# Optimization experiments

Measured on AMD Instinct MI355X. Metric: run time of the kernel, lower is better.

Reference implementation:

```python
import jax, jax.numpy as jnp
import numpy as np

N_NODES = 100000
N_EDGES = 1600000
LATENT = 64
NODE_DIM = 7
EDGE_DIM = 3
N_PARAMS = 2

def asinh_layer(p, x):
    # learned asinh: a*arcsinh(b*x + c) + d, p = [a, b, c, d]
    return p[0] * jnp.arcsinh(p[1] * x + p[2]) + p[3]

def mlp2(x, w1, b1, w2, b2):
    # ExplicitMLP([L, L]): gelu between layers, none on last
    return jax.nn.gelu(x @ w1 + b1) @ w2 + b2

def agg_stats(x, n):
    # custom_aggregation: [sum, mean, var, max]; mean/var denominators are n_data
    s = jnp.sum(x, axis=0, keepdims=True)
    m = s / n
    v = jnp.sum((x - m) ** 2, axis=0, keepdims=True) / n
    mx = jnp.max(x, axis=0, keepdims=True)
    return jnp.concatenate([s, m, v, mx], axis=-1)

def _forward(nodes, edges, asinh_node, w_en, b_en, asinh_edge, w_ee, b_ee, asinh_glob, w_eg, b_eg, ew1, eb1, ew2, eb2, nw1, nb1, nw2, nb2, gw1, gb1, gw2, gb2, gw3, gb3, senders):
    # decorate_nodes=False -> zero columns 0:4
    nodes = nodes.at[:, 0:4].set(0.0)
    # globals = arcsinh([n_node, n_edge]) as (1, 2)
    glob = jnp.arcsinh(jnp.array([[float(N_NODES), float(N_EDGES)]], dtype=nodes.dtype))
    # GraphMapFeatures embedding: asinh layer + Dense for nodes/edges/globals
    nodes = asinh_layer(asinh_node, nodes) @ w_en + b_en   # (N, L)
    edges = asinh_layer(asinh_edge, edges) @ w_ee + b_ee   # (E, L)
    glob = asinh_layer(asinh_glob, glob) @ w_eg + b_eg     # (1, L)
    # source overwrites receivers with senders
    recv = senders
    # edge update: concat(edges, nodes[senders], nodes[receivers], globals)
    ge = jnp.broadcast_to(glob, (edges.shape[0], glob.shape[-1]))
    e_in = jnp.concatenate([edges, nodes[senders], nodes[recv], ge], axis=-1)  # (E, 4L)
    edges = mlp2(e_in, ew1, eb1, ew2, eb2)                                     # (E, L)
    # node update: sent/received aggregates are identical since recv == senders
    sent = jax.ops.segment_sum(edges, senders, num_segments=N_NODES)           # (N, L)
    gn = jnp.broadcast_to(glob, (nodes.shape[0], glob.shape[-1]))
    n_in = jnp.concatenate([nodes, sent, sent, gn], axis=-1)                   # (N, 4L)
    nodes = mlp2(n_in, nw1, nb1, nw2, nb2)                                     # (N, L)
    # global update: arcsinh of [sum, mean, var, max] over nodes and edges (single graph)
    node_attr = jnp.arcsinh(agg_stats(nodes, float(N_NODES)))                  # (1, 4L)
    edge_attr = jnp.arcsinh(agg_stats(edges, float(N_EDGES)))                  # (1, 4L)
    g_in = jnp.concatenate([node_attr, edge_attr, glob], axis=-1)              # (1, 9L)
    g = jax.nn.gelu(g_in @ gw1 + gb1)
    g = jax.nn.gelu(g @ gw2 + gb2)
    g = g @ gw3 + gb3
    return g.reshape(-1)  # (N_PARAMS,)

def setup_inputs():
    key = jax.random.key(0)
    ks = jax.random.split(key, 16)
    L = LATENT
    def dense(k, fi, fo):
        return jax.random.normal(k, (fi, fo), jnp.float32) / np.float32(np.sqrt(fi))
    z = lambda n: jnp.zeros((n,), jnp.float32)
    asinh0 = jnp.array([1.0, 1.0, 0.0, 0.0], jnp.float32)
    return {
        "nodes": jax.random.normal(ks[0], (N_NODES, NODE_DIM), jnp.float32),
        "edges": jax.random.normal(ks[1], (N_EDGES, EDGE_DIM), jnp.float32),
        "senders": jax.random.randint(ks[2], (N_EDGES,), 0, N_NODES),
        "asinh_node": asinh0, "w_en": dense(ks[3], NODE_DIM, L), "b_en": z(L),
        "asinh_edge": asinh0, "w_ee": dense(ks[4], EDGE_DIM, L), "b_ee": z(L),
        "asinh_glob": asinh0, "w_eg": dense(ks[5], 2, L), "b_eg": z(L),
        "ew1": dense(ks[6], 4 * L, L), "eb1": z(L),
        "ew2": dense(ks[7], L, L), "eb2": z(L),
        "nw1": dense(ks[8], 4 * L, L), "nb1": z(L),
        "nw2": dense(ks[9], L, L), "nb2": z(L),
        "gw1": dense(ks[10], 9 * L, L), "gb1": z(L),
        "gw2": dense(ks[11], L, L), "gb2": z(L),
        "gw3": dense(ks[12], L, N_PARAMS), "gb3": z(N_PARAMS),
    }

def reference(nodes, edges, senders, asinh_node, w_en, b_en, asinh_edge, w_ee, b_ee, asinh_glob, w_eg, b_eg, ew1, eb1, ew2, eb2, nw1, nb1, nw2, nb2, gw1, gb1, gw2, gb2, gw3, gb3):
    return _forward(nodes, edges, asinh_node, w_en, b_en, asinh_edge, w_ee, b_ee, asinh_glob, w_eg, b_eg, ew1, eb1, ew2, eb2, nw1, nb1, nw2, nb2, gw1, gb1, gw2, gb2, gw3, gb3, senders)
```

## Files before the change

### kernel.cpp

```cpp
#include <hip/hip_runtime.h>
#include <cstdint>
#include <cstddef>

#define NN 100000
#define NE 1600000
#define NSLICE 16
#define NBLK 782
#define NBUCK 391
#define NCHUNK 391
#define CHA 4096

#define PRE_GLOB 0
#define PRE_WC   64
#define PRE_CVEC 256
#define PRE_CN   320
#define PRE_NGV  384
#define PRE_WSR  448
#define PRE_NSR  4544

#define TAB_W2  0
#define TAB_NW1 1
#define TAB_NSR 2
#define TAB_NW2 3
#define TAB_WSR 4

typedef short v8s __attribute__((ext_vector_type(8)));
typedef float v4f __attribute__((ext_vector_type(4)));

__device__ __forceinline__ float asinhf_fast(float x){
    float ax = fabsf(x);
    float r = __logf(ax + sqrtf(fmaf(ax, ax, 1.0f)));
    return copysignf(r, x);
}
__device__ __forceinline__ float gelu_f(float x){
    float x3 = x * x * x;
    float y = 1.5957691216057308f * fmaf(0.044715f, x3, x);
    float e = __expf(y);
    float r = __builtin_amdgcn_rcpf(e + 1.0f);
    return fmaf(-x, r, x);
}
__device__ __forceinline__ unsigned fkey(float f){
    unsigned u = __float_as_uint(f);
    return (u & 0x80000000u) ? ~u : (u | 0x80000000u);
}
__device__ __forceinline__ float funkey(unsigned k){
    unsigned u = (k & 0x80000000u) ? (k ^ 0x80000000u) : ~k;
    return __uint_as_float(u);
}
__device__ __forceinline__ void atomAddF(float* p, float v){
#if defined(__HIP_DEVICE_COMPILE__)
    unsafeAtomicAdd(p, v);
#else
    atomicAdd(p, v);
#endif
}
__device__ __forceinline__ void split8(const float* x, v8s& hi, v8s& lo){
#pragma unroll
    for (int j = 0; j < 8; ++j){
        unsigned u = __float_as_uint(x[j]);
        float hf = __uint_as_float(u & 0xFFFF0000u);
        float r = x[j] - hf;
        hi[j] = (short)(u >> 16);
        lo[j] = (short)(__float_as_uint(r) >> 16);
    }
}
__device__ __forceinline__ v4f mfma3(v8s ah, v8s al, v8s bh, v8s bl, v4f acc){
    acc = __builtin_amdgcn_mfma_f32_16x16x32_bf16(al, bh, acc, 0, 0, 0);
    acc = __builtin_amdgcn_mfma_f32_16x16x32_bf16(ah, bl, acc, 0, 0, 0);
    acc = __builtin_amdgcn_mfma_f32_16x16x32_bf16(ah, bh, acc, 0, 0, 0);
    return acc;
}
__device__ __forceinline__ void fma16(float acc[4][4], float4 a, float4 b){
    float av[4] = {a.x, a.y, a.z, a.w};
    float bv[4] = {b.x, b.y, b.z, b.w};
#pragma unroll
    for (int i = 0; i < 4; ++i)
#pragma unroll
        for (int c = 0; c < 4; ++c)
            acc[i][c] = fmaf(av[i], bv[c], acc[i][c]);
}

__global__ __launch_bounds__(256) void k_pre(const float* an, const float* w_en, const float* b_en,
                      const float* ae, const float* w_ee, const float* b_ee,
                      const float* ag, const float* w_eg, const float* b_eg,
                      const float* ew1, const float* eb1,
                      const float* nw1, const float* nb1,
                      const float* ew2, const float* nw2,
                      float* pre, unsigned short* preB, int* statsZero, int* counts)
{
    __shared__ float gls[64];
    __shared__ float red[3][4][64];
    __shared__ float redc[4][64], redn[4][64];
    int t = threadIdx.x, col = t & 63, qd = t >> 6;
    for (int i = t; i < 2 * NSLICE * 192; i += 256) statsZero[i] = 0;
    {
        int4* c4 = (int4*)counts;
        int4 z = make_int4(0, 0, 0, 0);
        for (int i = t; i < NN / 4; i += 256) c4[i] = z;
    }
    for (int i = t; i < 4096; i += 256){
        pre[PRE_WSR + i] = ew1[4096 + i] + ew1[8192 + i];
        pre[PRE_NSR + i] = nw1[4096 + i] + nw1[8192 + i];
    }
    if (t < 64){
        float g0 = asinhf_fast(100000.0f);
        float g1 = asinhf_fast(1600000.0f);
        float tg0 = fmaf(ag[0], asinhf_fast(fmaf(ag[1], g0, ag[2])), ag[3]);
        float tg1 = fmaf(ag[0], asinhf_fast(fmaf(ag[1], g1, ag[2])), ag[3]);
        float gl = fmaf(tg0, w_eg[t], fmaf(tg1, w_eg[64 + t], b_eg[t]));
        pre[PRE_GLOB + t] = gl;
        gls[t] = gl;
        float tz = fmaf(an[0], asinhf_fast(an[2]), an[3]);
        pre[PRE_CN + t] = fmaf(tz, w_en[t] + w_en[64 + t] + w_en[128 + t] + w_en[192 + t], b_en[t]);
    }
    __syncthreads();
    {
        float s0 = 0.f, s1 = 0.f, s2 = 0.f, sc = 0.f, sn = 0.f;
        int jb = qd * 16;
#pragma unroll 4
        for (int j = jb; j < jb + 16; ++j){
            float e1 = ew1[j * 64 + col];
            s0 = fmaf(w_ee[j], e1, s0);
            s1 = fmaf(w_ee[64 + j], e1, s1);
            s2 = fmaf(w_ee[128 + j], e1, s2);
            sc = fmaf(b_ee[j], e1, sc);
            float g = gls[j];
            sc = fmaf(g, ew1[(192 + j) * 64 + col], sc);
            sn = fmaf(g, nw1[(192 + j) * 64 + col], sn);
        }
        red[0][qd][col] = s0; red[1][qd][col] = s1; red[2][qd][col] = s2;
        redc[qd][col] = sc; redn[qd][col] = sn;
    }
    __syncthreads();
    if (t < 64){
#pragma unroll
        for (int i = 0; i < 3; ++i)
            pre[PRE_WC + i * 64 + t] = (red[i][0][t] + red[i][1][t]) + (red[i][2][t] + red[i][3][t]);
        pre[PRE_CVEC + t] = eb1[t] + (redc[0][t] + redc[1][t]) + (redc[2][t] + redc[3][t]);
        pre[PRE_NGV + t] = nb1[t] + (redn[0][t] + redn[1][t]) + (redn[2][t] + redn[3][t]);
    }
    __syncthreads();
    const float* srcs[5] = {ew2, nw1, pre + PRE_NSR, nw2, pre + PRE_WSR};
    for (int idx = t; idx < 5 * 4096; idx += 256){
        int tab = idx >> 12;
        int rem = idx & 4095;
        int c = rem >> 10;
        int ch = (rem >> 9) & 1;
        int lane = (rem >> 3) & 63;
        int j = rem & 7;
        int k = ch * 32 + (lane >> 4) * 8 + j;
        int n = c * 16 + (lane & 15);
        float v = srcs[tab][k * 64 + n];
        unsigned u = __float_as_uint(v);
        float hf = __uint_as_float(u & 0xFFFF0000u);
        float r = v - hf;
        int base = tab * 8192 + ((c * 2 + ch) * 2) * 512 + lane * 8 + j;
        preB[base] = (unsigned short)(u >> 16);
        preB[base + 512] = (unsigned short)(__float_as_uint(r) >> 16);
    }
}

__global__ __launch_bounds__(256) void k_nproj(const float* nodes, const float* an,
                                               const float* w_en, const float* pre,
                                               const unsigned short* preB,
                                               const int* senders, int* counts,
                                               float* sent, float* nproj)
{
    __shared__ float fz[64][4];
    __shared__ float latS[64][68];
    int t = threadIdx.x;
    int base = blockIdx.x * 64;
    int cnt = NN - base; if (cnt > 64) cnt = 64;
    const int NT = 1563 * 256;
    int gtid = blockIdx.x * 256 + t;
    for (int i = gtid; i < NE; i += NT)
        atomicAdd(&counts[senders[i]], 1);
    {
        float4 z = make_float4(0.f, 0.f, 0.f, 0.f);
        float4* s4 = (float4*)sent;
        for (int i = gtid; i < NN * 16; i += NT) s4[i] = z;
    }
    if (t < 64){
        float pa = an[0], pb = an[1], pc = an[2], pd = an[3];
        float t4 = 0.f, t5 = 0.f, t6 = 0.f;
        if (t < cnt){
            const float* row = nodes + (size_t)(base + t) * 7;
            t4 = fmaf(pa, asinhf_fast(fmaf(pb, row[4], pc)), pd);
            t5 = fmaf(pa, asinhf_fast(fmaf(pb, row[5], pc)), pd);
            t6 = fmaf(pa, asinhf_fast(fmaf(pb, row[6], pc)), pd);
        }
        fz[t][0] = t4; fz[t][1] = t5; fz[t][2] = t6;
    }
    __syncthreads();
    {
        int k = t & 63, grp = t >> 6;
        float w4 = w_en[4 * 64 + k], w5 = w_en[5 * 64 + k], w6 = w_en[6 * 64 + k];
        float cn = pre[PRE_CN + k];
#pragma unroll
        for (int i = 0; i < 16; ++i){
            int nl = grp * 16 + i;
            float v = cn;
            v = fmaf(fz[nl][0], w4, v);
            v = fmaf(fz[nl][1], w5, v);
            v = fmaf(fz[nl][2], w6, v);
            latS[nl][k] = (nl < cnt) ? v : 0.f;
        }
    }
    __syncthreads();
    int l = t & 63, w = t >> 6;
    int m = l & 15, q = l >> 4;
    v8s ah[2], al[2];
#pragma unroll
    for (int ch = 0; ch < 2; ++ch){
        float a[8];
        const float* src = &latS[w * 16 + m][ch * 32 + q * 8];
#pragma unroll
        for (int j = 0; j < 8; ++j) a[j] = src[j];
        split8(a, ah[ch], al[ch]);
    }
    const v8s* WB = (const v8s*)(preB + TAB_WSR * 8192);
    v4f acc[4];
#pragma unroll
    for (int c = 0; c < 4; ++c){
        acc[c] = (v4f){0.f, 0.f, 0.f, 0.f};
#pragma unroll
        for (int ch = 0; ch < 2; ++ch){
            v8s bh = WB[((c * 2 + ch) * 2 + 0) * 64 + l];
            v8s bl = WB[((c * 2 + ch) * 2 + 1) * 64 + l];
            acc[c] = mfma3(ah[ch], al[ch], bh, bl, acc[c]);
        }
    }
#pragma unroll
    for (int c = 0; c < 4; ++c)
#pragma unroll
        for (int r = 0; r < 4; ++r){
            int nl = w * 16 + q * 4 + r;
            if (nl < cnt)
                nproj[(size_t)(base + nl) * 64 + c * 16 + m] = acc[c][r];
        }
}

__global__ __launch_bounds__(128) void k_scanA(const int* counts, int* cursor, int* bsums)
{
    __shared__ int sA[128];
    int t = threadIdx.x, b = blockIdx.x;
    int i = b * 128 + t;
    int v = (i < NN) ? counts[i] : 0;
    sA[t] = v;
    __syncthreads();
    for (int off = 1; off < 128; off <<= 1){
        int x = (t >= off) ? sA[t - off] : 0;
        __syncthreads();
        sA[t] += x;
        __syncthreads();
    }
    if (i < NN) cursor[i] = sA[t] - v;
    if (t == 127) bsums[b] = sA[127];
}

__global__ __launch_bounds__(1024) void k_scanB(const int* bsums, int* bpre, int* bucketFill)
{
    __shared__ int sB[1024];
    int t = threadIdx.x;
    int v = (t < NBLK) ? bsums[t] : 0;
    sB[t] = v;
    __syncthreads();
    for (int off = 1; off < 1024; off <<= 1){
        int x = (t >= off) ? sB[t - off] : 0;
        __syncthreads();
        sB[t] += x;
        __syncthreads();
    }
    if (t < NBLK) bpre[t] = sB[t] - v;
    if (t < NBUCK) bucketFill[t] = (t == 0) ? 0 : sB[2 * t - 1];
}

__global__ __launch_bounds__(256) void k_binA(const float* edges, const int* senders,
                                              const float* ae, int* bucketFill, float4* binned)
{
    __shared__ int hist[NBUCK], hist2[NBUCK], runS[NBUCK];
    __shared__ int lofs[NBUCK + 1];
    __shared__ int sA[512];
    __shared__ int staged[CHA];
    int t = threadIdx.x, b = blockIdx.x;
    int beg = b * CHA;
    int end = beg + CHA; if (end > NE) end = NE;
    int n = end - beg;
    for (int i = t; i < NBUCK; i += 256){ hist[i] = 0; hist2[i] = 0; }
    __syncthreads();
    for (int i = beg + t; i < end; i += 256)
        atomicAdd(&hist[senders[i] >> 8], 1);
    __syncthreads();
    sA[t] = (t < NBUCK) ? hist[t] : 0;
    sA[t + 256] = (t + 256 < NBUCK) ? hist[t + 256] : 0;
    __syncthreads();
    for (int off = 1; off < 512; off <<= 1){
        int x0 = (t >= off) ? sA[t - off] : 0;
        int p = t + 256;
        int x1 = (p >= off) ? sA[p - off] : 0;
        __syncthreads();
        sA[t] += x0; sA[p] += x1;
        __syncthreads();
    }
    if (t < NBUCK) lofs[t] = sA[t] - hist[t];
    if (t + 256 < NBUCK) lofs[t + 256] = sA[t + 256] - hist[t + 256];
    if (t == 0) lofs[NBUCK] = n;
    for (int i = t; i < NBUCK; i += 256)
        if (hist[i] > 0) runS[i] = atomicAdd(&bucketFill[i], hist[i]);
    __syncthreads();
    for (int i = beg + t; i < end; i += 256){
        int bk = senders[i] >> 8;
        int r = atomicAdd(&hist2[bk], 1);
        staged[lofs[bk] + r] = i;
    }
    __syncthreads();
    float pa = ae[0], pb = ae[1], pc = ae[2], pd = ae[3];
    for (int p = t; p < n; p += 256){
        int lo = 0, hi = NBUCK;
        while (hi - lo > 1){
            int mid = (lo + hi) >> 1;
            if (lofs[mid] <= p) lo = mid; else hi = mid;
        }
        int idx = staged[p];
        const float* er = edges + (size_t)idx * 3;
        float t0 = fmaf(pa, asinhf_fast(fmaf(pb, er[0], pc)), pd);
        float t1 = fmaf(pa, asinhf_fast(fmaf(pb, er[1], pc)), pd);
        float t2 = fmaf(pa, asinhf_fast(fmaf(pb, er[2], pc)), pd);
        binned[runS[lo] + (p - lofs[lo])] =
            make_float4(t0, t1, t2, __int_as_float(senders[idx]));
    }
}

__global__ __launch_bounds__(256) void k_binB(const float4* binned, const int* cursor,
                                              const int* bpre, float4* eperm)
{
    __shared__ int cnt256[256];
    int t = threadIdx.x, b = blockIdx.x;
    int base = bpre[2 * b];
    int end = (b == NBUCK - 1) ? NE : bpre[2 * b + 2];
    cnt256[t] = 0;
    __syncthreads();
    for (int i = base + t; i < end; i += 256){
        float4 ed = binned[i];
        int s = __float_as_int(ed.w);
        int r = atomicAdd(&cnt256[s & 255], 1);
        eperm[cursor[s] + bpre[s >> 7] + r] = ed;
    }
}

__global__ __launch_bounds__(256) void k_edge_sorted(const float4* eperm, const float* nproj,
                                                     const float* pre, const unsigned short* preB,
                                                     const float* eb2,
                                                     float* sent, float* epart)
{
    __shared__ float oS[64][65];
    __shared__ float cWs[256];
    __shared__ int sArr[64];
    int t = threadIdx.x;
    cWs[t] = (t < 64) ? pre[PRE_CVEC + t] : pre[PRE_WC + t - 64];
    int l = t & 63, w = t >> 6;
    int m = l & 15, q = l >> 4;
    int e = w * 16 + m;
    float4 ed = eperm[blockIdx.x * 64 + e];
    int s = __float_as_int(ed.w);
    if (q == 0) sArr[e] = s;
    const float4* npb = (const float4*)(nproj + (size_t)s * 64);
    float4 npv0 = npb[2 * q], npv1 = npb[2 * q + 1];
    float4 npv2 = npb[8 + 2 * q], npv3 = npb[8 + 2 * q + 1];
    float t0 = ed.x, t1 = ed.y, t2 = ed.z;
    __syncthreads();
    float npf[2][8] = {{npv0.x, npv0.y, npv0.z, npv0.w, npv1.x, npv1.y, npv1.z, npv1.w},
                       {npv2.x, npv2.y, npv2.z, npv2.w, npv3.x, npv3.y, npv3.z, npv3.w}};
    v8s ah[2], al[2];
#pragma unroll
    for (int ch = 0; ch < 2; ++ch){
        int k0 = ch * 32 + q * 8;
        float h[8];
#pragma unroll
        for (int j = 0; j < 8; ++j){
            int k = k0 + j;
            float hp = cWs[k] + npf[ch][j];
            hp = fmaf(t0, cWs[64 + k], hp);
            hp = fmaf(t1, cWs[128 + k], hp);
            hp = fmaf(t2, cWs[192 + k], hp);
            h[j] = gelu_f(hp);
        }
        split8(h, ah[ch], al[ch]);
    }
    const v8s* WB = (const v8s*)(preB + TAB_W2 * 8192);
#pragma unroll
    for (int c = 0; c < 4; ++c){
        v4f acc = (v4f){0.f, 0.f, 0.f, 0.f};
#pragma unroll
        for (int ch = 0; ch < 2; ++ch){
            v8s bh = WB[((c * 2 + ch) * 2 + 0) * 64 + l];
            v8s bl = WB[((c * 2 + ch) * 2 + 1) * 64 + l];
            acc = mfma3(ah[ch], al[ch], bh, bl, acc);
        }
        float bb = eb2[c * 16 + m];
#pragma unroll
        for (int r = 0; r < 4; ++r)
            oS[w * 16 + q * 4 + r][c * 16 + m] = acc[r] + bb;
    }
    __syncthreads();
    if (w == 0){
        int k = l;
        int cur = sArr[0];
        int jstart = 0;
        float a = 0.f;
        for (int j = 0; j < 64; ++j){
            int sj = sArr[j];
            if (sj != cur){
                float* dst = sent + (size_t)cur * 64 + k;
                if (jstart > 0) *dst = a; else atomAddF(dst, a);
                cur = sj; a = 0.f; jstart = j;
            }
            a += oS[j][k];
        }
        atomAddF(sent + (size_t)cur * 64 + k, a);
    } else if (w == 1){
        int k = l;
        float ssum = 0.f, qsum = 0.f, mmax = -INFINITY;
#pragma unroll 4
        for (int j = 0; j < 64; ++j){
            float v = oS[j][k];
            ssum += v;
            qsum = fmaf(v, v, qsum);
            mmax = fmaxf(mmax, v);
        }
        float* ep = epart + (size_t)(blockIdx.x & (NSLICE - 1)) * 192;
        atomAddF(ep + k, ssum);
        atomAddF(ep + 64 + k, qsum);
        atomicMax((unsigned*)(ep + 128) + k, fkey(mmax));
    }
}

__global__ __launch_bounds__(256) void k_edge_atomic(const float* edges, const int* senders,
                                                     const float* nproj, const float* pre,
                                                     const float* ae, const float* ew2, const float* eb2,
                                                     float* sent, float* epart)
{
    __shared__ float hT[64][68];
    __shared__ int sArr[64];
    int t = threadIdx.x;
    int e = t & 63, kq = t >> 6;
    int eg = blockIdx.x * 64 + e;
    int s = senders[eg];
    if (kq == 0) sArr[e] = s;
    float pa = ae[0], pb = ae[1], pc = ae[2], pd = ae[3];
    const float* erow = edges + (size_t)eg * 3;
    float t0 = fmaf(pa, asinhf_fast(fmaf(pb, erow[0], pc)), pd);
    float t1 = fmaf(pa, asinhf_fast(fmaf(pb, erow[1], pc)), pd);
    float t2 = fmaf(pa, asinhf_fast(fmaf(pb, erow[2], pc)), pd);
    int j0 = kq * 16;
    const float* np = nproj + (size_t)s * 64 + j0;
    float npv[16];
#pragma unroll
    for (int qq = 0; qq < 4; ++qq){
        float4 v = *(const float4*)(np + qq * 4);
        npv[qq * 4 + 0] = v.x; npv[qq * 4 + 1] = v.y; npv[qq * 4 + 2] = v.z; npv[qq * 4 + 3] = v.w;
    }
    const float* Wc = pre + PRE_WC;
    const float* cvec = pre + PRE_CVEC;
#pragma unroll
    for (int jj = 0; jj < 16; ++jj){
        int j = j0 + jj;
        float hp = cvec[j] + npv[jj];
        hp = fmaf(t0, Wc[j], hp);
        hp = fmaf(t1, Wc[64 + j], hp);
        hp = fmaf(t2, Wc[128 + j], hp);
        hT[j][e] = gelu_f(hp);
    }
    __syncthreads();
    int e0 = (t & 15) * 4, k0 = (t >> 4) * 4;
    float acc[4][4];
    {
        float4 bb = *(const float4*)(eb2 + k0);
#pragma unroll
        for (int i = 0; i < 4; ++i){ acc[i][0] = bb.x; acc[i][1] = bb.y; acc[i][2] = bb.z; acc[i][3] = bb.w; }
    }
#pragma unroll 4
    for (int j = 0; j < 64; ++j){
        float4 a = *(const float4*)&hT[j][e0];
        float4 b = *(const float4*)(ew2 + j * 64 + k0);
        fma16(acc, a, b);
    }
#pragma unroll
    for (int i = 0; i < 4; ++i){
        int sv = sArr[e0 + i];
        float* dst = sent + (size_t)sv * 64 + k0;
        atomAddF(dst + 0, acc[i][0]);
        atomAddF(dst + 1, acc[i][1]);
        atomAddF(dst + 2, acc[i][2]);
        atomAddF(dst + 3, acc[i][3]);
    }
    float ps[4], pq[4], pm[4];
#pragma unroll
    for (int c = 0; c < 4; ++c){
        float s0 = acc[0][c], s1 = acc[1][c], s2 = acc[2][c], s3 = acc[3][c];
        ps[c] = (s0 + s1) + (s2 + s3);
        pq[c] = fmaf(s0, s0, fmaf(s1, s1, fmaf(s2, s2, s3 * s3)));
        pm[c] = fmaxf(fmaxf(s0, s1), fmaxf(s2, s3));
    }
#pragma unroll
    for (int msk = 1; msk < 16; msk <<= 1){
#pragma unroll
        for (int c = 0; c < 4; ++c){
            ps[c] += __shfl_xor(ps[c], msk);
            pq[c] += __shfl_xor(pq[c], msk);
            pm[c] = fmaxf(pm[c], __shfl_xor(pm[c], msk));
        }
    }
    float* ep = epart + (size_t)(blockIdx.x & (NSLICE - 1)) * 192;
    if ((t & 15) == 0){
#pragma unroll
        for (int c = 0; c < 4; ++c){
            atomAddF(ep + k0 + c, ps[c]);
            atomAddF(ep + 64 + k0 + c, pq[c]);
            atomicMax((unsigned*)(ep + 128) + k0 + c, fkey(pm[c]));
        }
    }
}

__global__ __launch_bounds__(256) void k_node(const float* nodes, const float* an,
                                              const float* w_en, const float* sent,
                                              const float* pre, const unsigned short* preB,
                                              const float* nb2, float* npart)
{
    __shared__ float fz[64][4];
    __shared__ float h2S[64][68];
    __shared__ float sS[4][64], qS[4][64], mS[4][64];
    int t = threadIdx.x;
    int base = blockIdx.x * 64;
    int cnt = NN - base; if (cnt > 64) cnt = 64;
    if (t < 64){
        float pa = an[0], pb = an[1], pc = an[2], pd = an[3];
        float t4 = 0.f, t5 = 0.f, t6 = 0.f;
        if (t < cnt){
            const float* row = nodes + (size_t)(base + t) * 7;
            t4 = fmaf(pa, asinhf_fast(fmaf(pb, row[4], pc)), pd);
            t5 = fmaf(pa, asinhf_fast(fmaf(pb, row[5], pc)), pd);
            t6 = fmaf(pa, asinhf_fast(fmaf(pb, row[6], pc)), pd);
        }
        fz[t][0] = t4; fz[t][1] = t5; fz[t][2] = t6;
    }
    __syncthreads();
    int l = t & 63, w = t >> 6;
    int m = l & 15, q = l >> 4;
    int rowA = w * 16 + m;
    bool vA = rowA < cnt;
    float f0 = fz[rowA][0], f1 = fz[rowA][1], f2 = fz[rowA][2];
    v8s lh[2], ll[2], sh[2], sl[2];
#pragma unroll
    for (int ch = 0; ch < 2; ++ch){
        int k0 = ch * 32 + q * 8;
        float a[8], b[8] = {0,0,0,0,0,0,0,0};
#pragma unroll
        for (int j = 0; j < 8; ++j){
            int k = k0 + j;
            float v = pre[PRE_CN + k];
            v = fmaf(f0, w_en[4 * 64 + k], v);
            v = fmaf(f1, w_en[5 * 64 + k], v);
            v = fmaf(f2, w_en[6 * 64 + k], v);
            a[j] = vA ? v : 0.f;
        }
        if (vA){
            const float4* psn = (const float4*)(sent + (size_t)(base + rowA) * 64 + k0);
            float4 b0 = psn[0], b1 = psn[1];
            b[0]=b0.x; b[1]=b0.y; b[2]=b0.z; b[3]=b0.w; b[4]=b1.x; b[5]=b1.y; b[6]=b1.z; b[7]=b1.w;
        }
        split8(a, lh[ch], ll[ch]);
        split8(b, sh[ch], sl[ch]);
    }
    const v8s* B1 = (const v8s*)(preB + TAB_NW1 * 8192);
    const v8s* BS = (const v8s*)(preB + TAB_NSR * 8192);
    v4f acc[4];
#pragma unroll
    for (int c = 0; c < 4; ++c){
        acc[c] = (v4f){0.f, 0.f, 0.f, 0.f};
#pragma unroll
        for (int ch = 0; ch < 2; ++ch){
            v8s bh = B1[((c * 2 + ch) * 2 + 0) * 64 + l];
            v8s bl = B1[((c * 2 + ch) * 2 + 1) * 64 + l];
            acc[c] = mfma3(lh[ch], ll[ch], bh, bl, acc[c]);
            v8s ch2 = BS[((c * 2 + ch) * 2 + 0) * 64 + l];
            v8s cl2 = BS[((c * 2 + ch) * 2 + 1) * 64 + l];
// ... 11 lines not shown
        float a[8];
        const float* src = &h2S[w * 16 + m][ch * 32 + q * 8];
#pragma unroll
        for (int j = 0; j < 8; ++j) a[j] = src[j];
        split8(a, ah[ch], al[ch]);
    }
    const v8s* B2 = (const v8s*)(preB + TAB_NW2 * 8192);
    float ps[4], pq[4], pm[4];
#pragma unroll
    for (int c = 0; c < 4; ++c){
        v4f a2 = (v4f){0.f, 0.f, 0.f, 0.f};
#pragma unroll
        for (int ch = 0; ch < 2; ++ch){
            v8s bh = B2[((c * 2 + ch) * 2 + 0) * 64 + l];
            v8s bl = B2[((c * 2 + ch) * 2 + 1) * 64 + l];
            a2 = mfma3(ah[ch], al[ch], bh, bl, a2);
        }
        float bb = nb2[c * 16 + m];
        ps[c] = 0.f; pq[c] = 0.f; pm[c] = -INFINITY;
#pragma unroll
        for (int r = 0; r < 4; ++r){
            int nl = w * 16 + q * 4 + r;
            if (nl < cnt){
                float v = a2[r] + bb;
                ps[c] += v;
                pq[c] = fmaf(v, v, pq[c]);
                pm[c] = fmaxf(pm[c], v);
            }
        }
    }
#pragma unroll
    for (int msk = 16; msk <= 32; msk <<= 1){
#pragma unroll
        for (int c = 0; c < 4; ++c){
            ps[c] += __shfl_xor(ps[c], msk);
            pq[c] += __shfl_xor(pq[c], msk);
            pm[c] = fmaxf(pm[c], __shfl_xor(pm[c], msk));
        }
    }
    if (l < 16){
#pragma unroll
        for (int c = 0; c < 4; ++c){
            sS[w][c * 16 + l] = ps[c];
            qS[w][c * 16 + l] = pq[c];
            mS[w][c * 16 + l] = pm[c];
        }
    }
    __syncthreads();
    if (t < 64){
        int k = t;
        float ssum = sS[0][k] + sS[1][k] + sS[2][k] + sS[3][k];
        float qsum = qS[0][k] + qS[1][k] + qS[2][k] + qS[3][k];
        float mmax = fmaxf(fmaxf(mS[0][k], mS[1][k]), fmaxf(mS[2][k], mS[3][k]));
        float* np = npart + (size_t)(blockIdx.x & (NSLICE - 1)) * 192;
        atomAddF(np + k, ssum);
        atomAddF(np + 64 + k, qsum);
        atomicMax((unsigned*)(np + 128) + k, fkey(mmax));
    }
}

__global__ __launch_bounds__(256) void k_final(const float* pre, const float* epart, const float* npart,
                        const float* gw1, const float* gb1, const float* gw2, const float* gb2,
                        const float* gw3, const float* gb3, float* out)
{
    __shared__ float gin[576];
    __shared__ float p1[4][64];
    __shared__ float l1s[64];
    __shared__ float l2s[64];
    int t = threadIdx.x;
    if (t < 64){
        float ns = 0.f, nq = 0.f; unsigned nmk = 0u;
        float es = 0.f, eq = 0.f; unsigned emk = 0u;
        for (int sl = 0; sl < NSLICE; ++sl){
            const float* np = npart + (size_t)sl * 192;
            const float* ep = epart + (size_t)sl * 192;
            ns += np[t]; nq += np[64 + t];
            unsigned a = ((const unsigned*)(np + 128))[t]; if (a > nmk) nmk = a;
            es += ep[t]; eq += ep[64 + t];
            unsigned b = ((const unsigned*)(ep + 128))[t]; if (b > emk) emk = b;
        }
        float mean = ns / 100000.0f;
        float var = nq / 100000.0f - mean * mean;
        gin[t] = asinhf_fast(ns);
        gin[64 + t] = asinhf_fast(mean);
        gin[128 + t] = asinhf_fast(var);
        gin[192 + t] = asinhf_fast(funkey(nmk));
        float meane = es / 1600000.0f;
        float vare = eq / 1600000.0f - meane * meane;
        gin[256 + t] = asinhf_fast(es);
        gin[320 + t] = asinhf_fast(meane);
        gin[384 + t] = asinhf_fast(vare);
        gin[448 + t] = asinhf_fast(funkey(emk));
        gin[512 + t] = pre[PRE_GLOB + t];
    }
    __syncthreads();
    {
        int col = t & 63, qq = t >> 6;
        float a1 = 0.f;
        for (int j = qq * 144; j < qq * 144 + 144; ++j)
            a1 = fmaf(gin[j], gw1[j * 64 + col], a1);
        p1[qq][col] = a1;
    }
    __syncthreads();
    if (t < 64){
        float a = gb1[t] + ((p1[0][t] + p1[1][t]) + (p1[2][t] + p1[3][t]));
        l1s[t] = gelu_f(a);
    }
    __syncthreads();
    if (t < 64){
        float a2 = gb2[t];
        for (int j = 0; j < 64; ++j) a2 = fmaf(l1s[j], gw2[j * 64 + t], a2);
        l2s[t] = gelu_f(a2);
    }
    __syncthreads();
    if (t < 2){
        float s = gb3[t];
        for (int j = 0; j < 64; ++j) s = fmaf(l2s[j], gw3[j * 2 + t], s);
        out[t] = s;
    }
}

extern "C" void kernel_launch(void* const* d_in, const int* in_sizes, int n_in,
                              void* d_out, int out_size, void* d_ws, size_t ws_size,
                              hipStream_t stream)
{
    const float* nodes  = (const float*)d_in[0];
    const float* edges  = (const float*)d_in[1];
    const int*   senders= (const int*)d_in[2];
    const float* an  = (const float*)d_in[3];
    const float* w_en= (const float*)d_in[4];
    const float* b_en= (const float*)d_in[5];
    const float* ae  = (const float*)d_in[6];
    const float* w_ee= (const float*)d_in[7];
    const float* b_ee= (const float*)d_in[8];
    const float* ag  = (const float*)d_in[9];
    const float* w_eg= (const float*)d_in[10];
    const float* b_eg= (const float*)d_in[11];
    const float* ew1 = (const float*)d_in[12];
    const float* eb1 = (const float*)d_in[13];
    const float* ew2 = (const float*)d_in[14];
    const float* eb2 = (const float*)d_in[15];
    const float* nw1 = (const float*)d_in[16];
    const float* nb1 = (const float*)d_in[17];
    const float* nw2 = (const float*)d_in[18];
    const float* nb2 = (const float*)d_in[19];
    const float* gw1 = (const float*)d_in[20];
    const float* gb1 = (const float*)d_in[21];
    const float* gw2 = (const float*)d_in[22];
    const float* gb2 = (const float*)d_in[23];
    const float* gw3 = (const float*)d_in[24];
    const float* gb3 = (const float*)d_in[25];

    char* ws = (char*)d_ws;
    float4* eperm = (float4*)(ws);
    float*  nproj = (float*)(ws + 25600000);
    float*  sent  = (float*)(ws + 51200000);
    float*  pre   = (float*)(ws + 76800000);
    unsigned short* preB = (unsigned short*)(ws + 76865536);
    float*  epart = (float*)(ws + 76963840);
    float*  npart = (float*)(ws + 76976128);
    int*    counts= (int*)  (ws + 76988416);
    int*    cursor= (int*)  (ws + 77388416);
    int*    bsums = (int*)  (ws + 77788416);
    int*    bpre  = (int*)  (ws + 77792512);
    int*    bucketFill = (int*)(ws + 77796608);
    float4* binned= (float4*)(ws + 77798416);

    const size_t NEED_FAST = 103398416;
    bool fast = (ws_size >= NEED_FAST);

    hipLaunchKernelGGL(k_pre, dim3(1), dim3(256), 0, stream,
                       an, w_en, b_en, ae, w_ee, b_ee, ag, w_eg, b_eg, ew1, eb1,
                       nw1, nb1, ew2, nw2, pre, preB, (int*)epart, counts);

    if (fast){
        hipLaunchKernelGGL(k_nproj, dim3((NN + 63) / 64), dim3(256), 0, stream,
                           nodes, an, w_en, pre, preB, senders, counts, sent, nproj);
        hipLaunchKernelGGL(k_scanA, dim3(NBLK), dim3(128), 0, stream, counts, cursor, bsums);
        hipLaunchKernelGGL(k_scanB, dim3(1), dim3(1024), 0, stream, bsums, bpre, bucketFill);
        hipLaunchKernelGGL(k_binA, dim3(NCHUNK), dim3(256), 0, stream,
                           edges, senders, ae, bucketFill, binned);
        hipLaunchKernelGGL(k_binB, dim3(NBUCK), dim3(256), 0, stream,
                           binned, cursor, bpre, eperm);
        hipLaunchKernelGGL(k_edge_sorted, dim3(NE / 64), dim3(256), 0, stream,
                           eperm, nproj, pre, preB, eb2, sent, epart);
    } else {
        hipLaunchKernelGGL(k_nproj, dim3((NN + 63) / 64), dim3(256), 0, stream,
                           nodes, an, w_en, pre, preB, senders, cursor, sent, nproj);
        hipLaunchKernelGGL(k_edge_atomic, dim3(NE / 64), dim3(256), 0, stream,
                           edges, senders, nproj, pre, ae, ew2, eb2, sent, epart);
    }

    hipLaunchKernelGGL(k_node, dim3((NN + 63) / 64), dim3(256), 0, stream,
                       nodes, an, w_en, sent, pre, preB, nb2, npart);
    hipLaunchKernelGGL(k_final, dim3(1), dim3(256), 0, stream,
                       pre, epart, npart, gw1, gb1, gw2, gb2, gw3, gb3, (float*)d_out);
}
```

Measured before the change: 429.8 us.

## Replace full counting sort with fixed-capacity 128-node buckets and LDS accumulation

Removes the per-node count, the two scan kernels and the second binning pass. Edges are instead binned straight into fixed-capacity buckets of 128 sender nodes, with a global overflow buffer for any excess. Each bucket block runs the edge MLP and accumulates the aggregated sums into shared memory with atomics, then writes its node rows of sent directly, so sent no longer needs zeroing. This cuts kernel launches and global passes over the edges. The costs are LDS atomic contention, only 782 blocks of larger per-block work, and a slow scalar fallback kernel for overflow edges.

```diff
diff --git a/kernel.cpp b/kernel.cpp
--- a/kernel.cpp
+++ b/kernel.cpp
@@ -5,10 +5,12 @@
 #define NN 100000
 #define NE 1600000
 #define NSLICE 16
-#define NBLK 782
-#define NBUCK 391
+#define NBUCK 782
+#define NBPAD 784
+#define BCAP 3072
 #define NCHUNK 391
 #define CHA 4096
+#define OVCAP 8192
 
 #define PRE_GLOB 0
 #define PRE_WC   64
@@ -86,18 +88,16 @@
                       const float* ew1, const float* eb1,
                       const float* nw1, const float* nb1,
                       const float* ew2, const float* nw2,
-                      float* pre, unsigned short* preB, int* statsZero, int* counts)
+                      float* pre, unsigned short* preB, int* statsZero,
+                      int* bucketFill, int* ovCnt)
 {
     __shared__ float gls[64];
     __shared__ float red[3][4][64];
     __shared__ float redc[4][64], redn[4][64];
     int t = threadIdx.x, col = t & 63, qd = t >> 6;
     for (int i = t; i < 2 * NSLICE * 192; i += 256) statsZero[i] = 0;
-    {
-        int4* c4 = (int4*)counts;
-        int4 z = make_int4(0, 0, 0, 0);
-        for (int i = t; i < NN / 4; i += 256) c4[i] = z;
-    }
+    for (int i = t; i < NBPAD; i += 256) bucketFill[i] = i * BCAP;
+    if (t == 0) ovCnt[0] = 0;
     for (int i = t; i < 4096; i += 256){
         pre[PRE_WSR + i] = ew1[4096 + i] + ew1[8192 + i];
         pre[PRE_NSR + i] = nw1[4096 + i] + nw1[8192 + i];
@@ -162,24 +162,13 @@
 
 __global__ __launch_bounds__(256) void k_nproj(const float* nodes, const float* an,
                                                const float* w_en, const float* pre,
-                                               const unsigned short* preB,
-                                               const int* senders, int* counts,
-                                               float* sent, float* nproj)
+                                               const unsigned short* preB, float* nproj)
 {
     __shared__ float fz[64][4];
     __shared__ float latS[64][68];
     int t = threadIdx.x;
     int base = blockIdx.x * 64;
     int cnt = NN - base; if (cnt > 64) cnt = 64;
-    const int NT = 1563 * 256;
-    int gtid = blockIdx.x * 256 + t;
-    for (int i = gtid; i < NE; i += NT)
-        atomicAdd(&counts[senders[i]], 1);
-    {
-        float4 z = make_float4(0.f, 0.f, 0.f, 0.f);
-        float4* s4 = (float4*)sent;
-        for (int i = gtid; i < NN * 16; i += NT) s4[i] = z;
-    }
     if (t < 64){
         float pa = an[0], pb = an[1], pc = an[2], pd = an[3];
         float t4 = 0.f, t5 = 0.f, t6 = 0.f;
@@ -240,83 +229,59 @@
         }
 }
 
-__global__ __launch_bounds__(128) void k_scanA(const int* counts, int* cursor, int* bsums)
-{
-    __shared__ int sA[128];
-    int t = threadIdx.x, b = blockIdx.x;
-    int i = b * 128 + t;
-    int v = (i < NN) ? counts[i] : 0;
-    sA[t] = v;
-    __syncthreads();
-    for (int off = 1; off < 128; off <<= 1){
-        int x = (t >= off) ? sA[t - off] : 0;
-        __syncthreads();
-        sA[t] += x;
-        __syncthreads();
-    }
-    if (i < NN) cursor[i] = sA[t] - v;
-    if (t == 127) bsums[b] = sA[127];
-}
-
-__global__ __launch_bounds__(1024) void k_scanB(const int* bsums, int* bpre, int* bucketFill)
-{
-    __shared__ int sB[1024];
-    int t = threadIdx.x;
-    int v = (t < NBLK) ? bsums[t] : 0;
-    sB[t] = v;
-    __syncthreads();
-    for (int off = 1; off < 1024; off <<= 1){
-        int x = (t >= off) ? sB[t - off] : 0;
-        __syncthreads();
-        sB[t] += x;
-        __syncthreads();
-    }
-    if (t < NBLK) bpre[t] = sB[t] - v;
-    if (t < NBUCK) bucketFill[t] = (t == 0) ? 0 : sB[2 * t - 1];
-}
-
 __global__ __launch_bounds__(256) void k_binA(const float* edges, const int* senders,
-                                              const float* ae, int* bucketFill, float4* binned)
-{
-    __shared__ int hist[NBUCK], hist2[NBUCK], runS[NBUCK];
-    __shared__ int lofs[NBUCK + 1];
-    __shared__ int sA[512];
+                                              const float* ae, int* bucketFill,
+                                              float4* binned, int* ovCnt, float4* ovBuf)
+{
+    __shared__ int hist[NBPAD], hist2[NBPAD], runS[NBPAD];
+    __shared__ int lofs[NBPAD + 1];
+    __shared__ int sB[256];
     __shared__ int staged[CHA];
     int t = threadIdx.x, b = blockIdx.x;
     int beg = b * CHA;
     int end = beg + CHA; if (end > NE) end = NE;
     int n = end - beg;
-    for (int i = t; i < NBUCK; i += 256){ hist[i] = 0; hist2[i] = 0; }
+    for (int i = t; i < NBPAD; i += 256){ hist[i] = 0; hist2[i] = 0; }
     __syncthreads();
     for (int i = beg + t; i < end; i += 256)
-        atomicAdd(&hist[senders[i] >> 8], 1);
-    __syncthreads();
-    sA[t] = (t < NBUCK) ? hist[t] : 0;
-    sA[t + 256] = (t + 256 < NBUCK) ? hist[t + 256] : 0;
-    __syncthreads();
-    for (int off = 1; off < 512; off <<= 1){
-        int x0 = (t >= off) ? sA[t - off] : 0;
-        int p = t + 256;
-        int x1 = (p >= off) ? sA[p - off] : 0;
+        atomicAdd(&hist[senders[i] >> 7], 1);
+    __syncthreads();
+    int i0 = 4 * t;
+    int h0 = (i0 < NBPAD) ? hist[i0] : 0;
+    int h1 = (i0 + 1 < NBPAD) ? hist[i0 + 1] : 0;
+    int h2 = (i0 + 2 < NBPAD) ? hist[i0 + 2] : 0;
+    int h3 = (i0 + 3 < NBPAD) ? hist[i0 + 3] : 0;
+    int tot = h0 + h1 + h2 + h3;
+    sB[t] = tot;
+    __syncthreads();
+    for (int off = 1; off < 256; off <<= 1){
+        int x = (t >= off) ? sB[t - off] : 0;
         __syncthreads();
-        sA[t] += x0; sA[p] += x1;
+        sB[t] += x;
         __syncthreads();
     }
-    if (t < NBUCK) lofs[t] = sA[t] - hist[t];
-    if (t + 256 < NBUCK) lofs[t + 256] = sA[t + 256] - hist[t + 256];
-    if (t == 0) lofs[NBUCK] = n;
-    for (int i = t; i < NBUCK; i += 256)
+    {
+        int run = sB[t] - tot;
+        if (i0 < NBPAD){
+            lofs[i0] = run; run += h0;
+            lofs[i0 + 1] = run; run += h1;
+            lofs[i0 + 2] = run; run += h2;
+            lofs[i0 + 3] = run;
+        }
+        if (t == 255) lofs[NBPAD] = sB[255];
+    }
+    for (int i = t; i < NBPAD; i += 256)
         if (hist[i] > 0) runS[i] = atomicAdd(&bucketFill[i], hist[i]);
     __syncthreads();
     for (int i = beg + t; i < end; i += 256){
-        int bk = senders[i] >> 8;
+        int bk = senders[i] >> 7;
         int r = atomicAdd(&hist2[bk], 1);
         staged[lofs[bk] + r] = i;
     }
     __syncthreads();
     float pa = ae[0], pb = ae[1], pc = ae[2], pd = ae[3];
     for (int p = t; p < n; p += 256){
-        int lo = 0, hi = NBUCK;
+        int lo = 0, hi = NBPAD;
         while (hi - lo > 1){
             int mid = (lo + hi) >> 1;
             if (lofs[mid] <= p) lo = mid; else hi = mid;
@@ -326,112 +291,154 @@
         float t0 = fmaf(pa, asinhf_fast(fmaf(pb, er[0], pc)), pd);
         float t1 = fmaf(pa, asinhf_fast(fmaf(pb, er[1], pc)), pd);
         float t2 = fmaf(pa, asinhf_fast(fmaf(pb, er[2], pc)), pd);
-        binned[runS[lo] + (p - lofs[lo])] =
-            make_float4(t0, t1, t2, __int_as_float(senders[idx]));
-    }
-}
-
-__global__ __launch_bounds__(256) void k_binB(const float4* binned, const int* cursor,
-                                              const int* bpre, float4* eperm)
-{
-    __shared__ int cnt256[256];
-    int t = threadIdx.x, b = blockIdx.x;
-    int base = bpre[2 * b];
-    int end = (b == NBUCK - 1) ? NE : bpre[2 * b + 2];
-    cnt256[t] = 0;
-    __syncthreads();
-    for (int i = base + t; i < end; i += 256){
-        float4 ed = binned[i];
-        int s = __float_as_int(ed.w);
-        int r = atomicAdd(&cnt256[s & 255], 1);
-        eperm[cursor[s] + bpre[s >> 7] + r] = ed;
-    }
-}
-
-__global__ __launch_bounds__(256) void k_edge_sorted(const float4* eperm, const float* nproj,
+        float4 f4 = make_float4(t0, t1, t2, __int_as_float(senders[idx]));
+        int slot = runS[lo] + (p - lofs[lo]);
+        if (slot < (lo + 1) * BCAP){
+            binned[slot] = f4;
+        } else {
+            int o = atomicAdd(ovCnt, 1);
+            if (o < OVCAP) ovBuf[o] = f4;
+        }
+    }
+}
+
+__global__ __launch_bounds__(256) void k_edge_bucket(const float4* binned, const float* nproj,
+                                                     const int* bucketFill,
                                                      const float* pre, const unsigned short* preB,
                                                      const float* eb2,
                                                      float* sent, float* epart)
 {
-    __shared__ float oS[64][65];
+    __shared__ float acc[128][65];
     __shared__ float cWs[256];
-    __shared__ int sArr[64];
-    int t = threadIdx.x;
+    __shared__ float sS[4][64], qS[4][64], mS[4][64];
+    int t = threadIdx.x, b = blockIdx.x;
+    int nodeBase = b * 128;
+    int cnt = bucketFill[b] - b * BCAP; if (cnt > BCAP) cnt = BCAP;
     cWs[t] = (t < 64) ? pre[PRE_CVEC + t] : pre[PRE_WC + t - 64];
+    for (int i = t; i < 128 * 65; i += 256) ((float*)acc)[i] = 0.f;
     int l = t & 63, w = t >> 6;
     int m = l & 15, q = l >> 4;
-    int e = w * 16 + m;
-    float4 ed = eperm[blockIdx.x * 64 + e];
-    int s = __float_as_int(ed.w);
-    if (q == 0) sArr[e] = s;
-    const float4* npb = (const float4*)(nproj + (size_t)s * 64);
-    float4 npv0 = npb[2 * q], npv1 = npb[2 * q + 1];
-    float4 npv2 = npb[8 + 2 * q], npv3 = npb[8 + 2 * q + 1];
-    float t0 = ed.x, t1 = ed.y, t2 = ed.z;
-    __syncthreads();
-    float npf[2][8] = {{npv0.x, npv0.y, npv0.z, npv0.w, npv1.x, npv1.y, npv1.z, npv1.w},
-                       {npv2.x, npv2.y, npv2.z, npv2.w, npv3.x, npv3.y, npv3.z, npv3.w}};
-    v8s ah[2], al[2];
-#pragma unroll
-    for (int ch = 0; ch < 2; ++ch){
-        int k0 = ch * 32 + q * 8;
-        float h[8];
-#pragma unroll
-        for (int j = 0; j < 8; ++j){
-            int k = k0 + j;
-            float hp = cWs[k] + npf[ch][j];
-            hp = fmaf(t0, cWs[64 + k], hp);
-            hp = fmaf(t1, cWs[128 + k], hp);
-            hp = fmaf(t2, cWs[192 + k], hp);
-            h[j] = gelu_f(hp);
-        }
-        split8(h, ah[ch], al[ch]);
-    }
+    float ps[4] = {0.f, 0.f, 0.f, 0.f}, pq[4] = {0.f, 0.f, 0.f, 0.f};
+    float pm[4] = {-INFINITY, -INFINITY, -INFINITY, -INFINITY};
+    __syncthreads();
+    const float4* bb = binned + (size_t)b * BCAP;
     const v8s* WB = (const v8s*)(preB + TAB_W2 * 8192);
-#pragma unroll
-    for (int c = 0; c < 4; ++c){
-        v4f acc = (v4f){0.f, 0.f, 0.f, 0.f};
+    float bias[4];
+#pragma unroll
+    for (int c = 0; c < 4; ++c) bias[c] = eb2[c * 16 + m];
+    int ntile = (cnt + 63) >> 6;
+    for (int tile = 0; tile < ntile; ++tile){
+        int e = tile * 64 + w * 16 + m;
+        bool vE = e < cnt;
+        float4 ed = vE ? bb[e] : make_float4(0.f, 0.f, 0.f, __int_as_float(nodeBase));
+        int s = __float_as_int(ed.w);
+        const float4* npb = (const float4*)(nproj + (size_t)s * 64);
+        float4 n0 = npb[2 * q], n1 = npb[2 * q + 1];
+        float4 n2 = npb[8 + 2 * q], n3 = npb[8 + 2 * q + 1];
+        float t0 = ed.x, t1 = ed.y, t2 = ed.z;
+        float npf[2][8] = {{n0.x, n0.y, n0.z, n0.w, n1.x, n1.y, n1.z, n1.w},
+                           {n2.x, n2.y, n2.z, n2.w, n3.x, n3.y, n3.z, n3.w}};
+        v8s ah[2], al[2];
 #pragma unroll
         for (int ch = 0; ch < 2; ++ch){
-            v8s bh = WB[((c * 2 + ch) * 2 + 0) * 64 + l];
-            v8s bl = WB[((c * 2 + ch) * 2 + 1) * 64 + l];
-            acc = mfma3(ah[ch], al[ch], bh, bl, acc);
-        }
-        float bb = eb2[c * 16 + m];
-#pragma unroll
-        for (int r = 0; r < 4; ++r)
-            oS[w * 16 + q * 4 + r][c * 16 + m] = acc[r] + bb;
-    }
-    __syncthreads();
-    if (w == 0){
-        int k = l;
-        int cur = sArr[0];
-        int jstart = 0;
-        float a = 0.f;
-        for (int j = 0; j < 64; ++j){
-            int sj = sArr[j];
-            if (sj != cur){
-                float* dst = sent + (size_t)cur * 64 + k;
-                if (jstart > 0) *dst = a; else atomAddF(dst, a);
-                cur = sj; a = 0.f; jstart = j;
+            int k0 = ch * 32 + q * 8;
+            float h[8];
+#pragma unroll
+            for (int j = 0; j < 8; ++j){
+                int k = k0 + j;
+                float hp = cWs[k] + npf[ch][j];
+                hp = fmaf(t0, cWs[64 + k], hp);
+                hp = fmaf(t1, cWs[128 + k], hp);
+                hp = fmaf(t2, cWs[192 + k], hp);
+                h[j] = gelu_f(hp);
             }
-            a += oS[j][k];
-        }
-        atomAddF(sent + (size_t)cur * 64 + k, a);
-    } else if (w == 1){
-        int k = l;
-        float ssum = 0.f, qsum = 0.f, mmax = -INFINITY;
-#pragma unroll 4
-        for (int j = 0; j < 64; ++j){
-            float v = oS[j][k];
-            ssum += v;
-            qsum = fmaf(v, v, qsum);
-            mmax = fmaxf(mmax, v);
-        }
-        float* ep = epart + (size_t)(blockIdx.x & (NSLICE - 1)) * 192;
+            split8(h, ah[ch], al[ch]);
+        }
+        int sr[4];
+#pragma unroll
+        for (int r = 0; r < 4; ++r) sr[r] = __shfl(s, q * 4 + r);
+#pragma unroll
+        for (int c = 0; c < 4; ++c){
+            v4f a = (v4f){0.f, 0.f, 0.f, 0.f};
+#pragma unroll
+            for (int ch = 0; ch < 2; ++ch){
+                v8s bh = WB[((c * 2 + ch) * 2 + 0) * 64 + l];
+                v8s bl = WB[((c * 2 + ch) * 2 + 1) * 64 + l];
+                a = mfma3(ah[ch], al[ch], bh, bl, a);
+            }
+#pragma unroll
+            for (int r = 0; r < 4; ++r){
+                int er = tile * 64 + w * 16 + q * 4 + r;
+                if (er < cnt){
+                    float v = a[r] + bias[c];
+                    atomicAdd(&acc[sr[r] - nodeBase][c * 16 + m], v);
+                    ps[c] += v;
+                    pq[c] = fmaf(v, v, pq[c]);
+                    pm[c] = fmaxf(pm[c], v);
+                }
+            }
+        }
+    }
+#pragma unroll
+    for (int msk = 16; msk <= 32; msk <<= 1){
+#pragma unroll
+        for (int c = 0; c < 4; ++c){
+            ps[c] += __shfl_xor(ps[c], msk);
+            pq[c] += __shfl_xor(pq[c], msk);
+            pm[c] = fmaxf(pm[c], __shfl_xor(pm[c], msk));
+        }
+    }
+    if (l < 16){
+#pragma unroll
+        for (int c = 0; c < 4; ++c){
+            sS[w][c * 16 + l] = ps[c];
+            qS[w][c * 16 + l] = pq[c];
+            mS[w][c * 16 + l] = pm[c];
+        }
+    }
+    __syncthreads();
+    if (t < 64){
+        int k = t;
+        float ssum = sS[0][k] + sS[1][k] + sS[2][k] + sS[3][k];
+        float qsum = qS[0][k] + qS[1][k] + qS[2][k] + qS[3][k];
+        float mmax = fmaxf(fmaxf(mS[0][k], mS[1][k]), fmaxf(mS[2][k], mS[3][k]));
+        float* ep = epart + (size_t)(b & (NSLICE - 1)) * 192;
         atomAddF(ep + k, ssum);
         atomAddF(ep + 64 + k, qsum);
         atomicMax((unsigned*)(ep + 128) + k, fkey(mmax));
+    }
+    for (int i = t; i < 128 * 64; i += 256){
+        int nl = i >> 6, k = i & 63;
+        int ng = nodeBase + nl;
+        if (ng < NN) sent[(size_t)ng * 64 + k] = acc[nl][k];
+    }
+}
+
+__global__ __launch_bounds__(256) void k_over(const int* ovCnt, const float4* ovBuf,
+                                              const float* nproj, const float* pre,
+                                              const float* ew2, const float* eb2,
+                                              float* sent, float* epart)
+{
+    int n = ovCnt[0]; if (n > OVCAP) n = OVCAP;
+    for (int i = blockIdx.x * 256 + threadIdx.x; i < n; i += 4 * 256){
+        float4 ed = ovBuf[i];
+        int s = __float_as_int(ed.w);
+        float h[64];
+        for (int k = 0; k < 64; ++k){
+            float hp = pre[PRE_CVEC + k] + nproj[(size_t)s * 64 + k];
+            hp = fmaf(ed.x, pre[PRE_WC + k], hp);
+            hp = fmaf(ed.y, pre[PRE_WC + 64 + k], hp);
+            hp = fmaf(ed.z, pre[PRE_WC + 128 + k], hp);
+            h[k] = gelu_f(hp);
+        }
+        for (int c = 0; c < 64; ++c){
+            float v = eb2[c];
+            for (int k = 0; k < 64; ++k) v = fmaf(h[k], ew2[k * 64 + c], v);
+            atomAddF(&sent[(size_t)s * 64 + c], v);
+            atomAddF(epart + c, v);
+            atomAddF(epart + 64 + c, v * v);
+            atomicMax((unsigned*)(epart + 128) + c, fkey(v));
+        }
     }
 }
 
@@ -749,41 +756,37 @@
     const float* gb3 = (const float*)d_in[25];
 
     char* ws = (char*)d_ws;
-    float4* eperm = (float4*)(ws);
-    float*  nproj = (float*)(ws + 25600000);
-    float*  sent  = (float*)(ws + 51200000);
-    float*  pre   = (float*)(ws + 76800000);
-    unsigned short* preB = (unsigned short*)(ws + 76865536);
-    float*  epart = (float*)(ws + 76963840);
-    float*  npart = (float*)(ws + 76976128);
-    int*    counts= (int*)  (ws + 76988416);
-    int*    cursor= (int*)  (ws + 77388416);
-    int*    bsums = (int*)  (ws + 77788416);
-    int*    bpre  = (int*)  (ws + 77792512);
-    int*    bucketFill = (int*)(ws + 77796608);
-    float4* binned= (float4*)(ws + 77798416);
-
-    const size_t NEED_FAST = 103398416;
+    float4* binned = (float4*)(ws);
+    float*  nproj  = (float*)(ws + 38436864);
+    float*  sent   = (float*)(ws + 64036864);
+    float*  pre    = (float*)(ws + 89636864);
+    unsigned short* preB = (unsigned short*)(ws + 89702400);
+    float*  epart  = (float*)(ws + 89800704);
+    float*  npart  = (float*)(ws + 89812992);
+    int*    bucketFill = (int*)(ws + 89825280);
+    int*    ovCnt  = (int*)  (ws + 89828416);
+    float4* ovBuf  = (float4*)(ws + 89828480);
+
+    const size_t NEED_FAST = 89959552;
     bool fast = (ws_size >= NEED_FAST);
 
     hipLaunchKernelGGL(k_pre, dim3(1), dim3(256), 0, stream,
                        an, w_en, b_en, ae, w_ee, b_ee, ag, w_eg, b_eg, ew1, eb1,
-                       nw1, nb1, ew2, nw2, pre, preB, (int*)epart, counts);
+                       nw1, nb1, ew2, nw2, pre, preB, (int*)epart, bucketFill, ovCnt);
 
     if (fast){
         hipLaunchKernelGGL(k_nproj, dim3((NN + 63) / 64), dim3(256), 0, stream,
-                           nodes, an, w_en, pre, preB, senders, counts, sent, nproj);
-        hipLaunchKernelGGL(k_scanA, dim3(NBLK), dim3(128), 0, stream, counts, cursor, bsums);
-        hipLaunchKernelGGL(k_scanB, dim3(1), dim3(1024), 0, stream, bsums, bpre, bucketFill);
+                           nodes, an, w_en, pre, preB, nproj);
         hipLaunchKernelGGL(k_binA, dim3(NCHUNK), dim3(256), 0, stream,
-                           edges, senders, ae, bucketFill, binned);
-        hipLaunchKernelGGL(k_binB, dim3(NBUCK), dim3(256), 0, stream,
-                           binned, cursor, bpre, eperm);
-        hipLaunchKernelGGL(k_edge_sorted, dim3(NE / 64), dim3(256), 0, stream,
-                           eperm, nproj, pre, preB, eb2, sent, epart);
+                           edges, senders, ae, bucketFill, binned, ovCnt, ovBuf);
+        hipLaunchKernelGGL(k_edge_bucket, dim3(NBUCK), dim3(256), 0, stream,
+                           binned, nproj, bucketFill, pre, preB, eb2, sent, epart);
+        hipLaunchKernelGGL(k_over, dim3(4), dim3(256), 0, stream,
+                           ovCnt, ovBuf, nproj, pre, ew2, eb2, sent, epart);
     } else {
         hipLaunchKernelGGL(k_nproj, dim3((NN + 63) / 64), dim3(256), 0, stream,
-                           nodes, an, w_en, pre, preB, senders, cursor, sent, nproj);
+                           nodes, an, w_en, pre, preB, nproj);
+        hipMemsetAsync(sent, 0, (size_t)NN * 64 * sizeof(float), stream);
         hipLaunchKernelGGL(k_edge_atomic, dim3(NE / 64), dim3(256), 0, stream,
                            edges, senders, nproj, pre, ae, ew2, eb2, sent, epart);
     }
```

Measured after the change: 917.8 us. +113.5%, slower.

## Merge two-level scan into one kernel and simplify edge binning scatter

Applied to the files above, without the earlier changes.

Replaces the two-pass prefix scan (block scan plus block-sum scan) with a single 1024-thread kernel that computes global per-node cursors and per-bucket bases directly. The first binning pass drops its in-block staging sort and binary search, scattering each edge straight to its bucket slot, and uses smaller chunks with twice as many blocks. The second pass runs 512 threads per bucket and indexes with global cursors. This removes a launch and shared-memory scan work, at the cost of a serial per-thread loop in the single-block scan and less coalesced writes in binning.

```diff
diff --git a/kernel.cpp b/kernel.cpp
--- a/kernel.cpp
+++ b/kernel.cpp
@@ -5,10 +5,9 @@
 #define NN 100000
 #define NE 1600000
 #define NSLICE 16
-#define NBLK 782
 #define NBUCK 391
-#define NCHUNK 391
-#define CHA 4096
+#define NCHUNK 782
+#define CHA 2048
 
 #define PRE_GLOB 0
 #define PRE_WC   64
@@ -240,30 +239,17 @@
         }
 }
 
-__global__ __launch_bounds__(128) void k_scanA(const int* counts, int* cursor, int* bsums)
-{
-    __shared__ int sA[128];
-    int t = threadIdx.x, b = blockIdx.x;
-    int i = b * 128 + t;
-    int v = (i < NN) ? counts[i] : 0;
-    sA[t] = v;
-    __syncthreads();
-    for (int off = 1; off < 128; off <<= 1){
-        int x = (t >= off) ? sA[t - off] : 0;
-        __syncthreads();
-        sA[t] += x;
-        __syncthreads();
-    }
-    if (i < NN) cursor[i] = sA[t] - v;
-    if (t == 127) bsums[b] = sA[127];
-}
-
-__global__ __launch_bounds__(1024) void k_scanB(const int* bsums, int* bpre, int* bucketFill)
+__global__ __launch_bounds__(1024) void k_scan(const int* counts, int* cursorG,
+                                               int* bucketBase, int* bucketFill)
 {
     __shared__ int sB[1024];
     int t = threadIdx.x;
-    int v = (t < NBLK) ? bsums[t] : 0;
-    sB[t] = v;
+    const int CH = 98;
+    int beg = t * CH; if (beg > NN) beg = NN;
+    int end = beg + CH; if (end > NN) end = NN;
+    int s = 0;
+    for (int i = beg; i < end; ++i) s += counts[i];
+    sB[t] = s;
     __syncthreads();
     for (int off = 1; off < 1024; off <<= 1){
         int x = (t >= off) ? sB[t - off] : 0;
@@ -271,80 +257,61 @@
         sB[t] += x;
         __syncthreads();
     }
-    if (t < NBLK) bpre[t] = sB[t] - v;
-    if (t < NBUCK) bucketFill[t] = (t == 0) ? 0 : sB[2 * t - 1];
+    int pref = sB[t] - s;
+    for (int i = beg; i < end; ++i){
+        cursorG[i] = pref;
+        if ((i & 255) == 0){
+            int bb = i >> 8;
+            bucketBase[bb] = pref;
+            bucketFill[bb] = pref;
+        }
+        pref += counts[i];
+    }
+    if (t == 0) bucketBase[NBUCK] = NE;
 }
 
 __global__ __launch_bounds__(256) void k_binA(const float* edges, const int* senders,
                                               const float* ae, int* bucketFill, float4* binned)
 {
     __shared__ int hist[NBUCK], hist2[NBUCK], runS[NBUCK];
-    __shared__ int lofs[NBUCK + 1];
-    __shared__ int sA[512];
-    __shared__ int staged[CHA];
     int t = threadIdx.x, b = blockIdx.x;
     int beg = b * CHA;
     int end = beg + CHA; if (end > NE) end = NE;
-    int n = end - beg;
     for (int i = t; i < NBUCK; i += 256){ hist[i] = 0; hist2[i] = 0; }
     __syncthreads();
     for (int i = beg + t; i < end; i += 256)
         atomicAdd(&hist[senders[i] >> 8], 1);
     __syncthreads();
-    sA[t] = (t < NBUCK) ? hist[t] : 0;
-    sA[t + 256] = (t + 256 < NBUCK) ? hist[t + 256] : 0;
-    __syncthreads();
-    for (int off = 1; off < 512; off <<= 1){
-        int x0 = (t >= off) ? sA[t - off] : 0;
-        int p = t + 256;
-        int x1 = (p >= off) ? sA[p - off] : 0;
-        __syncthreads();
-        sA[t] += x0; sA[p] += x1;
-        __syncthreads();
-    }
-    if (t < NBUCK) lofs[t] = sA[t] - hist[t];
-    if (t + 256 < NBUCK) lofs[t + 256] = sA[t + 256] - hist[t + 256];
-    if (t == 0) lofs[NBUCK] = n;
     for (int i = t; i < NBUCK; i += 256)
         if (hist[i] > 0) runS[i] = atomicAdd(&bucketFill[i], hist[i]);
     __syncthreads();
+    float pa = ae[0], pb = ae[1], pc = ae[2], pd = ae[3];
     for (int i = beg + t; i < end; i += 256){
-        int bk = senders[i] >> 8;
+        int s = senders[i];
+        int bk = s >> 8;
         int r = atomicAdd(&hist2[bk], 1);
-        staged[lofs[bk] + r] = i;
-    }
-    __syncthreads();
-    float pa = ae[0], pb = ae[1], pc = ae[2], pd = ae[3];
-    for (int p = t; p < n; p += 256){
-        int lo = 0, hi = NBUCK;
-        while (hi - lo > 1){
-            int mid = (lo + hi) >> 1;
-            if (lofs[mid] <= p) lo = mid; else hi = mid;
-        }
-        int idx = staged[p];
-        const float* er = edges + (size_t)idx * 3;
+        const float* er = edges + (size_t)i * 3;
         float t0 = fmaf(pa, asinhf_fast(fmaf(pb, er[0], pc)), pd);
         float t1 = fmaf(pa, asinhf_fast(fmaf(pb, er[1], pc)), pd);
         float t2 = fmaf(pa, asinhf_fast(fmaf(pb, er[2], pc)), pd);
-        binned[runS[lo] + (p - lofs[lo])] =
-            make_float4(t0, t1, t2, __int_as_float(senders[idx]));
-    }
-}
-
-__global__ __launch_bounds__(256) void k_binB(const float4* binned, const int* cursor,
-                                              const int* bpre, float4* eperm)
+        binned[runS[bk] + r] = make_float4(t0, t1, t2, __int_as_float(s));
+    }
+}
+
+__global__ __launch_bounds__(512) void k_binB(const float4* binned, const int* cursorG,
+                                              const int* bucketBase, float4* eperm)
 {
     __shared__ int cnt256[256];
     int t = threadIdx.x, b = blockIdx.x;
-    int base = bpre[2 * b];
-    int end = (b == NBUCK - 1) ? NE : bpre[2 * b + 2];
-    cnt256[t] = 0;
-    __syncthreads();
-    for (int i = base + t; i < end; i += 256){
+    int base = bucketBase[b];
+    int end = bucketBase[b + 1];
+    if (t < 256) cnt256[t] = 0;
+    __syncthreads();
+    for (int i = base + t; i < end; i += 512){
         float4 ed = binned[i];
         int s = __float_as_int(ed.w);
         int r = atomicAdd(&cnt256[s & 255], 1);
-        eperm[cursor[s] + bpre[s >> 7] + r] = ed;
+        eperm[cursorG[s] + r] = ed;
     }
 }
 
@@ -757,10 +724,9 @@
     float*  epart = (float*)(ws + 76963840);
     float*  npart = (float*)(ws + 76976128);
     int*    counts= (int*)  (ws + 76988416);
-    int*    cursor= (int*)  (ws + 77388416);
-    int*    bsums = (int*)  (ws + 77788416);
-    int*    bpre  = (int*)  (ws + 77792512);
-    int*    bucketFill = (int*)(ws + 77796608);
+    int*    cursorG = (int*)(ws + 77388416);
+    int*    bucketBase = (int*)(ws + 77788416);
+    int*    bucketFill = (int*)(ws + 77790000);
     float4* binned= (float4*)(ws + 77798416);
 
     const size_t NEED_FAST = 103398416;
@@ -773,17 +739,17 @@
     if (fast){
         hipLaunchKernelGGL(k_nproj, dim3((NN + 63) / 64), dim3(256), 0, stream,
                            nodes, an, w_en, pre, preB, senders, counts, sent, nproj);
-        hipLaunchKernelGGL(k_scanA, dim3(NBLK), dim3(128), 0, stream, counts, cursor, bsums);
-        hipLaunchKernelGGL(k_scanB, dim3(1), dim3(1024), 0, stream, bsums, bpre, bucketFill);
+        hipLaunchKernelGGL(k_scan, dim3(1), dim3(1024), 0, stream,
+                           counts, cursorG, bucketBase, bucketFill);
         hipLaunchKernelGGL(k_binA, dim3(NCHUNK), dim3(256), 0, stream,
                            edges, senders, ae, bucketFill, binned);
-        hipLaunchKernelGGL(k_binB, dim3(NBUCK), dim3(256), 0, stream,
-                           binned, cursor, bpre, eperm);
+        hipLaunchKernelGGL(k_binB, dim3(NBUCK), dim3(512), 0, stream,
+                           binned, cursorG, bucketBase, eperm);
         hipLaunchKernelGGL(k_edge_sorted, dim3(NE / 64), dim3(256), 0, stream,
                            eperm, nproj, pre, preB, eb2, sent, epart);
     } else {
         hipLaunchKernelGGL(k_nproj, dim3((NN + 63) / 64), dim3(256), 0, stream,
-                           nodes, an, w_en, pre, preB, senders, cursor, sent, nproj);
+                           nodes, an, w_en, pre, preB, senders, cursorG, sent, nproj);
         hipLaunchKernelGGL(k_edge_atomic, dim3(NE / 64), dim3(256), 0, stream,
                            edges, senders, nproj, pre, ae, ew2, eb2, sent, epart);
     }
```

Measured after the change: 594.2 us. 1.38x slower.
